# Kernel optimization log

Measured on AMD Instinct MI355X. Metric: run time of the kernel, lower is better.

## Reference

```python
import jax, jax.numpy as jnp
import numpy as np

N_NODES = 100000
N_CLASSES = 16


def _graph_conv(x, W, b, src, dst, n_nodes):
    # DGL GraphConv norm='both': D_out^{-1/2} on src, aggregate, D_in^{-1/2} on dst.
    ones = jnp.ones(src.shape[0], x.dtype)
    deg_out = jnp.clip(jax.ops.segment_sum(ones, src, num_segments=n_nodes), 1.0)
    deg_in = jnp.clip(jax.ops.segment_sum(ones, dst, num_segments=n_nodes), 1.0)
    h = (x * jax.lax.rsqrt(deg_out)[:, None]) @ W          # [N, out] project first (in>=out)
    agg = jax.ops.segment_sum(h[src], dst, num_segments=n_nodes)  # gather-scatter
    return agg * jax.lax.rsqrt(deg_in)[:, None] + b


def _hetero_conv(x, W, b, edge_src, edge_dst, n_nodes):
    # HeteroGraphConv(aggregate='sum') over R relations, each its own GraphConv.
    out = _graph_conv(x, W[0], b[0], edge_src[0], edge_dst[0], n_nodes)
    for r in range(1, W.shape[0]):
        out = out + _graph_conv(x, W[r], b[r], edge_src[r], edge_dst[r], n_nodes)
    return out


def reference(x, W0, b0, W_mu, b_mu, W_ls, b_ls, edge_src, edge_dst,
              pos_src, pos_dst, neg_src, neg_dst):
    n = x.shape[0]
    h1 = jax.nn.relu(_hetero_conv(x, W0, b0, edge_src, edge_dst, n))
    mean = _hetero_conv(h1, W_mu, b_mu, edge_src, edge_dst, n)
    log_std = _hetero_conv(h1, W_ls, b_ls, edge_src, edge_dst, n)
    noise = jax.random.normal(jax.random.key(42), mean.shape, mean.dtype)
    h = mean + noise * jnp.exp(log_std)                     # VGAE reparameterization
    pos_score = jnp.sum(h[pos_src] * h[pos_dst], axis=-1, keepdims=True)  # u_dot_v
    neg_score = jnp.sum(h[neg_src] * h[neg_dst], axis=-1, keepdims=True)
    return pos_score, neg_score, h


def setup_inputs() -> dict:
    key = jax.random.key(0)
    ks = jax.random.split(key, 12)
    R, E, EP = 3, 1600000, 500000
    in_f, hid, out = 128, 64, N_CLASSES
    return {
        "x": jax.random.normal(ks[0], (N_NODES, in_f), jnp.float32),
        "W0": jax.random.normal(ks[1], (R, in_f, hid), jnp.float32) * (1.0 / np.sqrt(in_f)),
        "b0": jnp.zeros((R, hid), jnp.float32),
        "W_mu": jax.random.normal(ks[2], (R, hid, out), jnp.float32) * (1.0 / np.sqrt(hid)),
        "b_mu": jnp.zeros((R, out), jnp.float32),
        "W_ls": jax.random.normal(ks[3], (R, hid, out), jnp.float32) * (1.0 / np.sqrt(hid)),
        "b_ls": jnp.zeros((R, out), jnp.float32),
        "edge_src": jax.random.randint(ks[4], (R, E), 0, N_NODES, jnp.int32),
        "edge_dst": jax.random.randint(ks[5], (R, E), 0, N_NODES, jnp.int32),
        "pos_src": jax.random.randint(ks[6], (EP,), 0, N_NODES, jnp.int32),
        "pos_dst": jax.random.randint(ks[7], (EP,), 0, N_NODES, jnp.int32),
        "neg_src": jax.random.randint(ks[8], (EP,), 0, N_NODES, jnp.int32),
        "neg_dst": jax.random.randint(ks[9], (EP,), 0, N_NODES, jnp.int32),
    }
```

## Files before the change

kernel.cpp:

```cpp
#include <hip/hip_runtime.h>
#include <math.h>

#define N_NODES 100000
#define NREL 3
#define E_PER 1600000
#define E_TOT 4800000
#define EP 500000
#define F_IN 128
#define F_HID 64
#define F_OUT 16
#define NRN 300000

#define NSEG 7
#define SEGSZ 16000
#define NBLK 32
#define CHUNK (E_PER / NBLK)
#define SEGO 25000
#define NSEGO 4

#define OFF_DOUT    0
#define OFF_DINVIN  300000
#define OFF_CNT     600000
#define OFF_G       900000
#define OFF_BSUM    1200000
#define OFF_CSR     1201024
#define OFF_ESLOT   6001024
#define OFF_HPROJ   6001024
#define OFF_H1      12401088
#define OFF_HP22    18801088
#define WS_NEED_CSR 22001120
#define HP2SZ 3200032
#define ODINV_OUT 0
#define ODINV_IN  300000
#define OH1ACC    600000
#define OHPROJ    7000000
#define OL2ACC    13400000

__device__ __forceinline__ float atomAddF(float* p, float v) {
    return unsafeAtomicAdd(p, v);
}

__device__ __forceinline__ unsigned rotl32(unsigned x, unsigned d) {
    return (x << d) | (x >> (32u - d));
}

__device__ float jax_noise(unsigned i) {
    const unsigned ks0 = 0u, ks1 = 42u;
    const unsigned ks2 = ks0 ^ ks1 ^ 0x1BD11BDAu;
    unsigned x0 = 0u + ks0;
    unsigned x1 = i + ks1;
#define TFR(r) { x0 += x1; x1 = rotl32(x1, r); x1 ^= x0; }
    TFR(13) TFR(15) TFR(26) TFR(6)
    x0 += ks1; x1 += ks2 + 1u;
    TFR(17) TFR(29) TFR(16) TFR(24)
    x0 += ks2; x1 += ks0 + 2u;
    TFR(13) TFR(15) TFR(26) TFR(6)
    x0 += ks0; x1 += ks1 + 3u;
    TFR(17) TFR(29) TFR(16) TFR(24)
    x0 += ks1; x1 += ks2 + 4u;
    TFR(13) TFR(15) TFR(26) TFR(6)
    x0 += ks2; x1 += ks0 + 5u;
#undef TFR
    const unsigned bits = x0 ^ x1;
    float f = __uint_as_float((bits >> 9) | 0x3f800000u) - 1.0f;
    const float lo = -0.99999994f;
    float u = fmaxf(lo, f * 2.0f + lo);
    float w = -log1pf(-u * u);
    float p;
    if (w < 5.0f) {
        w -= 2.5f;
        p = 2.81022636e-08f;
        p = fmaf(p, w, 3.43273939e-07f);
        p = fmaf(p, w, -3.5233877e-06f);
        p = fmaf(p, w, -4.39150654e-06f);
        p = fmaf(p, w, 0.00021858087f);
        p = fmaf(p, w, -0.00125372503f);
        p = fmaf(p, w, -0.00417768164f);
        p = fmaf(p, w, 0.246640727f);
        p = fmaf(p, w, 1.50140941f);
    } else {
        w = sqrtf(w) - 3.0f;
        p = -0.000200214257f;
        p = fmaf(p, w, 0.000100950558f);
        p = fmaf(p, w, 0.00134934322f);
        p = fmaf(p, w, -0.00367342844f);
        p = fmaf(p, w, 0.00573950773f);
        p = fmaf(p, w, -0.0076224613f);
        p = fmaf(p, w, 0.00943887047f);
        p = fmaf(p, w, 1.00167406f);
        p = fmaf(p, w, 2.83297682f);
    }
    return 1.41421356237f * (p * u);
}

__global__ __launch_bounds__(512) void k_histin(const int* __restrict__ ed,
                                                int* __restrict__ cnt,
                                                int* __restrict__ eslot) {
    __shared__ int lds[SEGSZ];
    const int r = blockIdx.z, g = blockIdx.y, b = blockIdx.x;
    const int lo = g * SEGSZ;
    const int hi = min(lo + SEGSZ, N_NODES);
    const int nbins = hi - lo;
    for (int i = threadIdx.x; i < nbins; i += 512) lds[i] = 0;
    __syncthreads();
    const int e0 = r * E_PER + b * CHUNK;
    const int e1 = e0 + CHUNK;
    for (int e = e0 + threadIdx.x * 4; e + 4 <= e1; e += 512 * 4) {
        const int4 d4 = *(const int4*)(ed + e);
        if (d4.x >= lo && d4.x < hi) atomicAdd(&lds[d4.x - lo], 1);
        if (d4.y >= lo && d4.y < hi) atomicAdd(&lds[d4.y - lo], 1);
        if (d4.z >= lo && d4.z < hi) atomicAdd(&lds[d4.z - lo], 1);
        if (d4.w >= lo && d4.w < hi) atomicAdd(&lds[d4.w - lo], 1);
    }
    __syncthreads();
    for (int i = threadIdx.x; i < nbins; i += 512) {
        const int c = lds[i];
        lds[i] = c ? atomicAdd(&cnt[r * N_NODES + lo + i], c) : 0;
    }
    __syncthreads();
    for (int e = e0 + threadIdx.x * 4; e + 4 <= e1; e += 512 * 4) {
        const int4 d4 = *(const int4*)(ed + e);
        if (d4.x >= lo && d4.x < hi) eslot[e]     = atomicAdd(&lds[d4.x - lo], 1);
        if (d4.y >= lo && d4.y < hi) eslot[e + 1] = atomicAdd(&lds[d4.y - lo], 1);
        if (d4.z >= lo && d4.z < hi) eslot[e + 2] = atomicAdd(&lds[d4.z - lo], 1);
        if (d4.w >= lo && d4.w < hi) eslot[e + 3] = atomicAdd(&lds[d4.w - lo], 1);
    }
}

__global__ __launch_bounds__(512) void k_histout(const int* __restrict__ es,
                                                 int* __restrict__ dout) {
    __shared__ int lds[SEGO / 2];
    const int r = blockIdx.z, g = blockIdx.y, b = blockIdx.x;
    const int lo = g * SEGO;
    const int hi = lo + SEGO;
    for (int i = threadIdx.x; i < SEGO / 2; i += 512) lds[i] = 0;
    __syncthreads();
    const int e0 = r * E_PER + b * CHUNK;
    const int e1 = e0 + CHUNK;
    for (int e = e0 + threadIdx.x * 4; e + 4 <= e1; e += 512 * 4) {
        const int4 s4 = *(const int4*)(es + e);
        if (s4.x >= lo && s4.x < hi) {
            const int i = s4.x - lo;
            atomicAdd(&lds[i >> 1], 1 << ((i & 1) * 16));
        }
        if (s4.y >= lo && s4.y < hi) {
            const int i = s4.y - lo;
            atomicAdd(&lds[i >> 1], 1 << ((i & 1) * 16));
        }
        if (s4.z >= lo && s4.z < hi) {
            const int i = s4.z - lo;
            atomicAdd(&lds[i >> 1], 1 << ((i & 1) * 16));
        }
        if (s4.w >= lo && s4.w < hi) {
            const int i = s4.w - lo;
            atomicAdd(&lds[i >> 1], 1 << ((i & 1) * 16));
        }
    }
    __syncthreads();
    for (int i = threadIdx.x; i < SEGO / 2; i += 512) {
        const unsigned c = (unsigned)lds[i];
        const int c0 = (int)(c & 0xffffu);
        const int c1 = (int)(c >> 16);
        if (c0) atomicAdd(&dout[r * N_NODES + lo + 2 * i], c0);
        if (c1) atomicAdd(&dout[r * N_NODES + lo + 2 * i + 1], c1);
    }
}

__global__ __launch_bounds__(256) void k_scanA(const int* __restrict__ cnt,
                                               int* __restrict__ bsum) {
    __shared__ int red[256];
    const int base = blockIdx.x * 1024 + threadIdx.x * 4;
    int s = 0;
#pragma unroll
    for (int q = 0; q < 4; ++q) {
        const int i = base + q;
        s += (i < NRN) ? cnt[i] : 0;
    }
    red[threadIdx.x] = s;
    __syncthreads();
    for (int w = 128; w > 0; w >>= 1) {
        if (threadIdx.x < w) red[threadIdx.x] += red[threadIdx.x + w];
        __syncthreads();
    }
    if (threadIdx.x == 0) bsum[blockIdx.x] = red[0];
}

__global__ __launch_bounds__(512) void k_scanB(int* __restrict__ bsum) {
    __shared__ int sc[512];
    const int t = threadIdx.x;
    sc[t] = (t < 294) ? bsum[t] : 0;
    __syncthreads();
    for (int o = 1; o < 512; o <<= 1) {
        const int v = (t >= o) ? sc[t - o] : 0;
        __syncthreads();
        sc[t] += v;
        __syncthreads();
    }
    bsum[t] = (t > 0) ? sc[t - 1] : 0;
}

__global__ __launch_bounds__(256) void k_scanC(const int* __restrict__ cnt,
                                               const int* __restrict__ bsum,
                                               int* __restrict__ G,
                                               float* __restrict__ dinv_in,
                                               int* doutc) {
    __shared__ int sc[256];
    const int t = threadIdx.x;
    const int base = blockIdx.x * 1024 + t * 4;
    int v[4];
    int ts = 0;
#pragma unroll
    for (int q = 0; q < 4; ++q) {
        const int i = base + q;
        v[q] = (i < NRN) ? cnt[i] : 0;
        ts += v[q];
    }
    sc[t] = ts;
    __syncthreads();
    for (int o = 1; o < 256; o <<= 1) {
        const int x = (t >= o) ? sc[t - o] : 0;
        __syncthreads();
        sc[t] += x;
        __syncthreads();
    }
    int run = bsum[blockIdx.x] + ((t > 0) ? sc[t - 1] : 0);
#pragma unroll
    for (int q = 0; q < 4; ++q) {
        const int i = base + q;
        if (i < NRN) {
            G[i] = run;
            dinv_in[i] = rsqrtf((float)max(v[q], 1));
            const int oc = doutc[i];
            ((float*)doutc)[i] = rsqrtf((float)max(oc, 1));
        }
        run += v[q];
    }
}

__global__ __launch_bounds__(256) void k_fill(const int* __restrict__ es,
                                              const int* __restrict__ ed,
                                              const int* __restrict__ eslot,
                                              const int* __restrict__ G,
                                              int* __restrict__ csr) {
    const int r = blockIdx.y;
    const int e = (blockIdx.x * 256 + threadIdx.x) * 4;
    if (e + 4 > E_PER) return;
    const int gid = r * E_PER + e;
    const int4 s4 = *(const int4*)(es + gid);
    const int4 d4 = *(const int4*)(ed + gid);
    const int4 l4 = *(const int4*)(eslot + gid);
    const int rb = r * N_NODES;
    csr[G[rb + d4.x] + l4.x] = s4.x;
    csr[G[rb + d4.y] + l4.y] = s4.y;
    csr[G[rb + d4.z] + l4.z] = s4.z;
    csr[G[rb + d4.w] + l4.w] = s4.w;
}

__global__ __launch_bounds__(256) void k_gather1(const float* __restrict__ hp,
                                                 const int* __restrict__ csr,
                                                 const int* __restrict__ G,
                                                 const float* __restrict__ dinv,
                                                 float* __restrict__ h1,
                                                 int rbase, int first) {
    const int node = (blockIdx.x * 256 + threadIdx.x) >> 6;
    const int lane = threadIdx.x & 63;
    const int l16 = lane & 15;
    const int e4 = lane >> 4;
    const int idx = rbase + node;
    const int off0 = G[idx];
    const int off1 = (idx == NRN - 1) ? E_TOT : G[idx + 1];
    float ax = 0.f, ay = 0.f, az = 0.f, aw = 0.f;
    for (int base = off0; base < off1; base += 64) {
        int m = off1 - base;
        if (m > 64) m = 64;
        const int sv = (lane < m) ? csr[base + lane] : N_NODES;
        const int nq = (m + 3) >> 2;
        for (int q = 0; q < nq; ++q) {
            const int ei = q * 4 + e4;
            const int s = __shfl(sv, ei);
            const float4 v = *(const float4*)(hp + (size_t)s * F_HID + l16 * 4);
            ax += v.x;
            ay += v.y;
            az += v.z;
            aw += v.w;
        }
    }
    ax += __shfl_xor(ax, 16); ay += __shfl_xor(ay, 16);
    az += __shfl_xor(az, 16); aw += __shfl_xor(aw, 16);
    ax += __shfl_xor(ax, 32); ay += __shfl_xor(ay, 32);
    az += __shfl_xor(az, 32); aw += __shfl_xor(aw, 32);
    if (lane < 16) {
        const float dv = dinv[idx];
        float4* dst = (float4*)(h1 + (size_t)node * F_HID) + l16;
        float4 o;
        if (first) {
            o.x = dv * ax; o.y = dv * ay; o.z = dv * az; o.w = dv * aw;
        } else {
            const float4 pr = *dst;
            o.x = pr.x + dv * ax; o.y = pr.y + dv * ay;
            o.z = pr.z + dv * az; o.w = pr.w + dv * aw;
        }
        *dst = o;
    }
}

__global__ __launch_bounds__(256) void k_gather2_all(const float* __restrict__ hp0,
                                                     const float* __restrict__ hp1,
                                                     const float* __restrict__ hp2,
                                                     const int* __restrict__ csr,
                                                     const int* __restrict__ G,
                                                     const float* __restrict__ dinv,
                                                     const float* __restrict__ bmu,
                                                     const float* __restrict__ bls,
                                                     float* __restrict__ outh) {
    const int node = (blockIdx.x * 256 + threadIdx.x) >> 4;
    const int lane = threadIdx.x & 63;
    const int gl = lane & 15;
    const int l8 = lane & 7;
    const int e2 = (lane >> 3) & 1;
    float ox = 0.f, oy = 0.f, oz = 0.f, ow = 0.f;
#pragma unroll
    for (int r = 0; r < NREL; ++r) {
        const float* hp = (r == 0) ? hp0 : (r == 1) ? hp1 : hp2;
        const int idx = r * N_NODES + node;
        const int off0 = G[idx];
        const int off1 = (idx == NRN - 1) ? E_TOT : G[idx + 1];
        const int deg = off1 - off0;
        float ax = 0.f, ay = 0.f, az = 0.f, aw = 0.f;
        for (int ei0 = 0; ei0 < deg; ei0 += 4) {
            const int eiA = ei0 + e2;
            const int eiB = ei0 + 2 + e2;
            const int sA = (eiA < deg) ? csr[off0 + eiA] : N_NODES;
            const int sB = (eiB < deg) ? csr[off0 + eiB] : N_NODES;
            const float4 vA = *(const float4*)(hp + (size_t)sA * 32 + l8 * 4);
            const float4 vB = *(const float4*)(hp + (size_t)sB * 32 + l8 * 4);
            ax += vA.x; ay += vA.y; az += vA.z; aw += vA.w;
            ax += vB.x; ay += vB.y; az += vB.z; aw += vB.w;
        }
        ax += __shfl_xor(ax, 8);
        ay += __shfl_xor(ay, 8);
        az += __shfl_xor(az, 8);
        aw += __shfl_xor(aw, 8);
        const float dv = dinv[idx];
        ox = fmaf(dv, ax, ox);
        oy = fmaf(dv, ay, oy);
        oz = fmaf(dv, az, oz);
        ow = fmaf(dv, aw, ow);
    }
    const int gb = lane & 48;
    const int srcM = gb + (gl >> 2);
    const int srcL = gb + 4 + (gl >> 2);
    const float m0 = __shfl(ox, srcM), m1 = __shfl(oy, srcM),
                m2 = __shfl(oz, srcM), m3 = __shfl(ow, srcM);
    const float s0 = __shfl(ox, srcL), s1 = __shfl(oy, srcL),
                s2 = __shfl(oz, srcL), s3 = __shfl(ow, srcL);
    const float mm = (gl & 2) ? ((gl & 1) ? m3 : m2) : ((gl & 1) ? m1 : m0);
    const float ss = (gl & 2) ? ((gl & 1) ? s3 : s2) : ((gl & 1) ? s1 : s0);
    const float mean = mm + bmu[gl] + bmu[16 + gl] + bmu[32 + gl];
    const float lstd = ss + bls[gl] + bls[16 + gl] + bls[32 + gl];
    outh[(size_t)node * 16 + gl] =
        mean + jax_noise((unsigned)(node * 16 + gl)) * expf(lstd);
}

__global__ __launch_bounds__(256) void k_project1(const float* __restrict__ x,
                                                  const float* __restrict__ W,
                                                  const float* __restrict__ dinv,
                                                  float* __restrict__ out) {
    __shared__ float ws[F_IN * F_HID];
    for (int i = threadIdx.x; i < F_IN * F_HID; i += 256) ws[i] = W[i];
    __syncthreads();
    for (int t = blockIdx.x * 256 + threadIdx.x; t < (N_NODES + 1) * 16;
         t += gridDim.x * 256) {
        const int n = t >> 4;
        const int c0 = (t & 15) << 2;
        const int nn = min(n, N_NODES - 1);
        const float4* xr = (const float4*)(x + (size_t)nn * F_IN);
        float a0 = 0.f, a1 = 0.f, a2 = 0.f, a3 = 0.f;
#pragma unroll 8
        for (int k4 = 0; k4 < F_IN / 4; ++k4) {
            const float4 xv = xr[k4];
            const float4 w0 = *(const float4*)(ws + (k4 * 4 + 0) * F_HID + c0);
            const float4 w1 = *(const float4*)(ws + (k4 * 4 + 1) * F_HID + c0);
            const float4 w2 = *(const float4*)(ws + (k4 * 4 + 2) * F_HID + c0);
            const float4 w3 = *(const float4*)(ws + (k4 * 4 + 3) * F_HID + c0);
            a0 = fmaf(xv.x, w0.x, a0); a1 = fmaf(xv.x, w0.y, a1);
            a2 = fmaf(xv.x, w0.z, a2); a3 = fmaf(xv.x, w0.w, a3);
            a0 = fmaf(xv.y, w1.x, a0); a1 = fmaf(xv.y, w1.y, a1);
            a2 = fmaf(xv.y, w1.z, a2); a3 = fmaf(xv.y, w1.w, a3);
            a0 = fmaf(xv.z, w2.x, a0); a1 = fmaf(xv.z, w2.y, a1);
            a2 = fmaf(xv.z, w2.z, a2); a3 = fmaf(xv.z, w2.w, a3);
            a0 = fmaf(xv.w, w3.x, a0); a1 = fmaf(xv.w, w3.y, a1);
            a2 = fmaf(xv.w, w3.z, a2); a3 = fmaf(xv.w, w3.w, a3);
        }
        const float dv = (n < N_NODES) ? dinv[nn] : 0.f;
        float4 o;
        o.x = a0 * dv; o.y = a1 * dv; o.z = a2 * dv; o.w = a3 * dv;
        *(float4*)(out + (size_t)n * F_HID + c0) = o;
    }
}

__global__ __launch_bounds__(256) void k_project2(const float* __restrict__ h1,
                                                  const float* __restrict__ b0,
                                                  const float* __restrict__ Wmu,
                                                  const float* __restrict__ Wls,
                                                  const float* __restrict__ dinv,
                                                  float* __restrict__ out) {
    __shared__ float ws[F_HID * 32];
    __shared__ float bs[F_HID];
    for (int i = threadIdx.x; i < F_HID * 32; i += 256) {
        const int k = i >> 5, c = i & 31;
        ws[i] = (c < 16) ? Wmu[k * 16 + c] : Wls[k * 16 + (c - 16)];
    }
    if (threadIdx.x < F_HID)
        bs[threadIdx.x] = b0[threadIdx.x] + b0[64 + threadIdx.x] + b0[128 + threadIdx.x];
    __syncthreads();
    for (int t = blockIdx.x * 256 + threadIdx.x; t < (N_NODES + 1) * 8;
         t += gridDim.x * 256) {
        const int n = t >> 3;
        const int c0 = (t & 7) << 2;
        const int nn = min(n, N_NODES - 1);
        const float4* hr = (const float4*)(h1 + (size_t)nn * F_HID);
        float a0 = 0.f, a1 = 0.f, a2 = 0.f, a3 = 0.f;
#pragma unroll 4
        for (int k4 = 0; k4 < F_HID / 4; ++k4) {
            const float4 hv = hr[k4];
            const float4 bv = *(const float4*)(bs + k4 * 4);
            const float r0 = fmaxf(hv.x + bv.x, 0.f);
            const float r1 = fmaxf(hv.y + bv.y, 0.f);
            const float r2 = fmaxf(hv.z + bv.z, 0.f);
            const float r3 = fmaxf(hv.w + bv.w, 0.f);
            const float4 w0 = *(const float4*)(ws + (k4 * 4 + 0) * 32 + c0);
            const float4 w1 = *(const float4*)(ws + (k4 * 4 + 1) * 32 + c0);
            const float4 w2 = *(const float4*)(ws + (k4 * 4 + 2) * 32 + c0);
            const float4 w3 = *(const float4*)(ws + (k4 * 4 + 3) * 32 + c0);
            a0 = fmaf(r0, w0.x, a0); a1 = fmaf(r0, w0.y, a1);
            a2 = fmaf(r0, w0.z, a2); a3 = fmaf(r0, w0.w, a3);
            a0 = fmaf(r1, w1.x, a0); a1 = fmaf(r1, w1.y, a1);
            a2 = fmaf(r1, w1.z, a2); a3 = fmaf(r1, w1.w, a3);
            a0 = fmaf(r2, w2.x, a0); a1 = fmaf(r2, w2.y, a1);
            a2 = fmaf(r2, w2.z, a2); a3 = fmaf(r2, w2.w, a3);
            a0 = fmaf(r3, w3.x, a0); a1 = fmaf(r3, w3.y, a1);
            a2 = fmaf(r3, w3.z, a2); a3 = fmaf(r3, w3.w, a3);
        }
        const float dv = (n < N_NODES) ? dinv[nn] : 0.f;
        float4 o;
        o.x = a0 * dv; o.y = a1 * dv; o.z = a2 * dv; o.w = a3 * dv;
        *(float4*)(out + (size_t)n * 32 + c0) = o;
    }
}

__global__ __launch_bounds__(256) void k_scores(const int* __restrict__ ps,
                                                const int* __restrict__ pd,
                                                const int* __restrict__ ns,
                                                const int* __restrict__ nd,
                                                const float* __restrict__ h,
                                                float* __restrict__ out) {
    const int i = blockIdx.x * 256 + threadIdx.x;
    if (i >= 2 * EP) return;
    const int j = (i < EP) ? i : i - EP;
    const int a = (i < EP) ? ps[j] : ns[j];
    const int b = (i < EP) ? pd[j] : nd[j];
    const float4* ha = (const float4*)(h + (size_t)a * 16);
    const float4* hb = (const float4*)(h + (size_t)b * 16);
    float s = 0.f;
#pragma unroll
    for (int q = 0; q < 4; ++q) {
        const float4 u = ha[q];
        const float4 v = hb[q];
        s += u.x * v.x + u.y * v.y + u.z * v.z + u.w * v.w;
    }
    out[i] = s;
}

__global__ __launch_bounds__(256) void k_degrees(const int* __restrict__ es,
                                                 const int* __restrict__ ed,
                                                 float* __restrict__ dout,
                                                 float* __restrict__ din) {
    const int r = blockIdx.y;
    const int e = blockIdx.x * 256 + threadIdx.x;
    const int s = es[r * E_PER + e];
    const int d = ed[r * E_PER + e];
    atomAddF(&dout[r * N_NODES + s], 1.0f);
    atomAddF(&din[r * N_NODES + d], 1.0f);
}

__global__ __launch_bounds__(256) void k_finalize_deg(float* __restrict__ d) {
    const int i = blockIdx.x * 256 + threadIdx.x;
    if (i < 2 * NRN) d[i] = 1.0f / sqrtf(fmaxf(d[i], 1.0f));
}

__global__ __launch_bounds__(256) void k_scatter1(const float* __restrict__ hp,
                                                  const int* __restrict__ es,
                                                  const int* __restrict__ ed,
                                                  const float* __restrict__ din,
                                                  float* __restrict__ acc) {
    const int t = blockIdx.x * 256 + threadIdx.x;
    const int e = t >> 6;
    const int lane = t & 63;
    const int s = es[e];
    const int d = ed[e];
    const float v = hp[s * F_HID + lane] * din[d];
    atomAddF(&acc[d * F_HID + lane], v);
}

__global__ __launch_bounds__(256) void k_scatter2(const float* __restrict__ hp,
                                                  const int* __restrict__ es,
                                                  const int* __restrict__ ed,
                                                  const float* __restrict__ din,
                                                  float* __restrict__ acc) {
    const int t = blockIdx.x * 256 + threadIdx.x;
    const int e = t >> 5;
    const int c = t & 31;
    const int s = es[e];
    const int d = ed[e];
    const float v = hp[s * 32 + c] * din[d];
    atomAddF(&acc[d * 32 + c], v);
}

__global__ __launch_bounds__(256) void k_finalize(const float* __restrict__ l2,
                                                  const float* __restrict__ bmu,
                                                  const float* __restrict__ bls,
                                                  float* __restrict__ outh) {
    const int i = blockIdx.x * 256 + threadIdx.x;
    const int n = i >> 4, c = i & 15;
    const float mean = l2[n * 32 + c] + bmu[c] + bmu[16 + c] + bmu[32 + c];
    const float lstd = l2[n * 32 + 16 + c] + bls[c] + bls[16 + c] + bls[32 + c];
    const float z = jax_noise((unsigned)i);
    outh[i] = mean + z * expf(lstd);
}

extern "C" void kernel_launch(void* const* d_in, const int* in_sizes, int n_in,
                              void* d_out, int out_size, void* d_ws, size_t ws_size,
                              hipStream_t stream) {
    const float* x   = (const float*)d_in[0];
    const float* W0  = (const float*)d_in[1];
    const float* b0  = (const float*)d_in[2];
    const float* Wmu = (const float*)d_in[3];
    const float* bmu = (const float*)d_in[4];
    const float* Wls = (const float*)d_in[5];
    const float* bls = (const float*)d_in[6];
    const int* es = (const int*)d_in[7];
    const int* ed = (const int*)d_in[8];
    const int* ps = (const int*)d_in[9];
    const int* pd = (const int*)d_in[10];
    const int* ns = (const int*)d_in[11];
    const int* nd = (const int*)d_in[12];
    float* out = (float*)d_out;
    float* wsf = (float*)d_ws;

    if (ws_size >= (size_t)WS_NEED_CSR * sizeof(float)) {
        int*   doutc   = (int*)(wsf + OFF_DOUT);
        float* doutf   = wsf + OFF_DOUT;
        float* dinv_in = wsf + OFF_DINVIN;
        int*   cnt     = (int*)(wsf + OFF_CNT);
        int*   G       = (int*)(wsf + OFF_G);
        int*   bsum    = (int*)(wsf + OFF_BSUM);
        int*   csr     = (int*)(wsf + OFF_CSR);
        int*   eslot   = (int*)(wsf + OFF_ESLOT);
        float* hproj   = wsf + OFF_HPROJ;
        float* hp20    = wsf + OFF_HPROJ;
        float* hp21    = wsf + OFF_HPROJ + HP2SZ;
        float* hp22    = wsf + OFF_HP22;
        float* h1acc   = wsf + OFF_H1;

        hipMemsetAsync(doutc, 0, (size_t)NRN * sizeof(int), stream);
        hipMemsetAsync(cnt, 0, (size_t)NRN * sizeof(int), stream);

        k_histin<<<dim3(NBLK, NSEG, NREL), 512, 0, stream>>>(ed, cnt, eslot);
        k_histout<<<dim3(NBLK, NSEGO, NREL), 512, 0, stream>>>(es, doutc);
        k_scanA<<<294, 256, 0, stream>>>(cnt, bsum);
        k_scanB<<<1, 512, 0, stream>>>(bsum);
        k_scanC<<<294, 256, 0, stream>>>(cnt, bsum, G, dinv_in, doutc);
        k_fill<<<dim3((E_PER / 4 + 255) / 256, NREL), 256, 0, stream>>>(
            es, ed, eslot, G, csr);

        for (int r = 0; r < NREL; ++r) {
            k_project1<<<1280, 256, 0, stream>>>(
                x, W0 + (size_t)r * F_IN * F_HID, doutf + (size_t)r * N_NODES, hproj);
            k_gather1<<<N_NODES / 4, 256, 0, stream>>>(
                hproj, csr, G, dinv_in, h1acc, r * N_NODES, r == 0);
        }
        float* hp2s[NREL] = {hp20, hp21, hp22};
        for (int r = 0; r < NREL; ++r) {
            k_project2<<<1024, 256, 0, stream>>>(
                h1acc, b0, Wmu + (size_t)r * F_HID * F_OUT,
                Wls + (size_t)r * F_HID * F_OUT, doutf + (size_t)r * N_NODES,
                hp2s[r]);
        }
        k_gather2_all<<<N_NODES / 16, 256, 0, stream>>>(
            hp20, hp21, hp22, csr, G, dinv_in, bmu, bls, out + 2 * EP);
        k_scores<<<(2 * EP + 255) / 256, 256, 0, stream>>>(
            ps, pd, ns, nd, out + 2 * EP, out);
    } else {
        float* dinv_out = wsf + ODINV_OUT;
        float* dinv_in  = wsf + ODINV_IN;
        float* h1acc    = wsf + OH1ACC;
        float* hproj    = wsf + OHPROJ;
        float* l2acc    = wsf + OL2ACC;

        hipMemsetAsync(dinv_out, 0, (size_t)2 * NRN * sizeof(float), stream);
        hipMemsetAsync(h1acc, 0, (size_t)N_NODES * F_HID * sizeof(float), stream);
        hipMemsetAsync(l2acc, 0, (size_t)N_NODES * 32 * sizeof(float), stream);

        k_degrees<<<dim3(E_PER / 256, NREL), 256, 0, stream>>>(es, ed, dinv_out, dinv_in);
        k_finalize_deg<<<(2 * NRN + 255) / 256, 256, 0, stream>>>(wsf);

        for (int r = 0; r < NREL; ++r) {
            k_project1<<<1280, 256, 0, stream>>>(
                x, W0 + (size_t)r * F_IN * F_HID, dinv_out + (size_t)r * N_NODES, hproj);
            k_scatter1<<<E_PER / 4, 256, 0, stream>>>(
                hproj, es + (size_t)r * E_PER, ed + (size_t)r * E_PER,
                dinv_in + (size_t)r * N_NODES, h1acc);
        }
        for (int r = 0; r < NREL; ++r) {
            k_project2<<<1024, 256, 0, stream>>>(
                h1acc, b0, Wmu + (size_t)r * F_HID * F_OUT,
                Wls + (size_t)r * F_HID * F_OUT, dinv_out + (size_t)r * N_NODES, hproj);
            k_scatter2<<<E_PER / 8, 256, 0, stream>>>(
                hproj, es + (size_t)r * E_PER, ed + (size_t)r * E_PER,
                dinv_in + (size_t)r * N_NODES, l2acc);
        }
        k_finalize<<<N_NODES * F_OUT / 256, 256, 0, stream>>>(
            l2acc, bmu, bls, out + 2 * EP);
        k_scores<<<(2 * EP + 255) / 256, 256, 0, stream>>>(
            ps, pd, ns, nd, out + 2 * EP, out);
    }
}
```

Measured before the change: 843.9 us.

## Fuse per-relation layer-2 projections, enlarge histogram segments, unroll gather2 loop

Replaces the three k_project2 launches with a single k_project2_all kernel. It reads each h1 row once and applies the ReLU+bias once for all three relations, cutting repeated h1 reads and launch overhead. The histogram kernels now use dynamic shared memory with larger segments, so fewer segments are needed and the edge arrays are rescanned fewer times, at some cost to occupancy. The gather2 inner loop is unrolled to four neighbour loads per step to raise memory-level parallelism, which also raises register pressure.

Result: faster. 792.7 us (-6.1%).

```diff
diff --git a/kernel.cpp b/kernel.cpp
--- a/kernel.cpp
+++ b/kernel.cpp
@@ -11,12 +11,12 @@
 #define F_OUT 16
 #define NRN 300000
 
-#define NSEG 7
-#define SEGSZ 16000
+#define NSEG 5
+#define SEGSZ 20000
 #define NBLK 32
 #define CHUNK (E_PER / NBLK)
-#define SEGO 25000
-#define NSEGO 4
+#define SEGO 40000
+#define NSEGO 3
 
 #define OFF_DOUT    0
 #define OFF_DINVIN  300000
@@ -96,7 +96,7 @@
 __global__ __launch_bounds__(512) void k_histin(const int* __restrict__ ed,
                                                 int* __restrict__ cnt,
                                                 int* __restrict__ eslot) {
-    __shared__ int lds[SEGSZ];
+    extern __shared__ int lds[];
     const int r = blockIdx.z, g = blockIdx.y, b = blockIdx.x;
     const int lo = g * SEGSZ;
     const int hi = min(lo + SEGSZ, N_NODES);
@@ -129,11 +129,13 @@
 
 __global__ __launch_bounds__(512) void k_histout(const int* __restrict__ es,
                                                  int* __restrict__ dout) {
-    __shared__ int lds[SEGO / 2];
+    extern __shared__ int lds[];
     const int r = blockIdx.z, g = blockIdx.y, b = blockIdx.x;
     const int lo = g * SEGO;
-    const int hi = lo + SEGO;
-    for (int i = threadIdx.x; i < SEGO / 2; i += 512) lds[i] = 0;
+    const int hi = min(lo + SEGO, N_NODES);
+    const int nbins = hi - lo;
+    const int nwords = (nbins + 1) >> 1;
+    for (int i = threadIdx.x; i < nwords; i += 512) lds[i] = 0;
     __syncthreads();
     const int e0 = r * E_PER + b * CHUNK;
     const int e1 = e0 + CHUNK;
@@ -157,12 +159,13 @@
         }
     }
     __syncthreads();
-    for (int i = threadIdx.x; i < SEGO / 2; i += 512) {
+    for (int i = threadIdx.x; i < nwords; i += 512) {
         const unsigned c = (unsigned)lds[i];
         const int c0 = (int)(c & 0xffffu);
         const int c1 = (int)(c >> 16);
         if (c0) atomicAdd(&dout[r * N_NODES + lo + 2 * i], c0);
-        if (c1) atomicAdd(&dout[r * N_NODES + lo + 2 * i + 1], c1);
+        if (c1 && 2 * i + 1 < nbins)
+            atomicAdd(&dout[r * N_NODES + lo + 2 * i + 1], c1);
     }
 }
 
@@ -327,15 +330,23 @@
         const int off1 = (idx == NRN - 1) ? E_TOT : G[idx + 1];
         const int deg = off1 - off0;
         float ax = 0.f, ay = 0.f, az = 0.f, aw = 0.f;
-        for (int ei0 = 0; ei0 < deg; ei0 += 4) {
+        for (int ei0 = 0; ei0 < deg; ei0 += 8) {
             const int eiA = ei0 + e2;
             const int eiB = ei0 + 2 + e2;
+            const int eiC = ei0 + 4 + e2;
+            const int eiD = ei0 + 6 + e2;
             const int sA = (eiA < deg) ? csr[off0 + eiA] : N_NODES;
             const int sB = (eiB < deg) ? csr[off0 + eiB] : N_NODES;
+            const int sC = (eiC < deg) ? csr[off0 + eiC] : N_NODES;
+            const int sD = (eiD < deg) ? csr[off0 + eiD] : N_NODES;
             const float4 vA = *(const float4*)(hp + (size_t)sA * 32 + l8 * 4);
             const float4 vB = *(const float4*)(hp + (size_t)sB * 32 + l8 * 4);
+            const float4 vC = *(const float4*)(hp + (size_t)sC * 32 + l8 * 4);
+            const float4 vD = *(const float4*)(hp + (size_t)sD * 32 + l8 * 4);
             ax += vA.x; ay += vA.y; az += vA.z; aw += vA.w;
             ax += vB.x; ay += vB.y; az += vB.z; aw += vB.w;
+            ax += vC.x; ay += vC.y; az += vC.z; aw += vC.w;
+            ax += vD.x; ay += vD.y; az += vD.z; aw += vD.w;
         }
         ax += __shfl_xor(ax, 8);
         ay += __shfl_xor(ay, 8);
@@ -396,6 +407,78 @@
         float4 o;
         o.x = a0 * dv; o.y = a1 * dv; o.z = a2 * dv; o.w = a3 * dv;
         *(float4*)(out + (size_t)n * F_HID + c0) = o;
+    }
+}
+
+__global__ __launch_bounds__(256) void k_project2_all(const float* __restrict__ h1,
+                                                      const float* __restrict__ b0,
+                                                      const float* __restrict__ Wmu,
+                                                      const float* __restrict__ Wls,
+                                                      const float* __restrict__ dinv,
+                                                      float* __restrict__ o0,
+                                                      float* __restrict__ o1,
+                                                      float* __restrict__ o2) {
+    __shared__ float ws[NREL * F_HID * 32];
+    __shared__ float bs[F_HID];
+    for (int i = threadIdx.x; i < NREL * F_HID * 32; i += 256) {
+        const int r = i >> 11;
+        const int j = i & 2047;
+        const int k = j >> 5, c = j & 31;
+        ws[i] = (c < 16) ? Wmu[r * F_HID * 16 + k * 16 + c]
+                         : Wls[r * F_HID * 16 + k * 16 + (c - 16)];
+    }
+    if (threadIdx.x < F_HID)
+        bs[threadIdx.x] = b0[threadIdx.x] + b0[64 + threadIdx.x] + b0[128 + threadIdx.x];
+    __syncthreads();
+    for (int t = blockIdx.x * 256 + threadIdx.x; t < (N_NODES + 1) * 8;
+         t += gridDim.x * 256) {
+        const int n = t >> 3;
+        const int c0 = (t & 7) << 2;
+        const int nn = min(n, N_NODES - 1);
+        const float4* hr = (const float4*)(h1 + (size_t)nn * F_HID);
+        float a00 = 0.f, a01 = 0.f, a02 = 0.f, a03 = 0.f;
+        float a10 = 0.f, a11 = 0.f, a12 = 0.f, a13 = 0.f;
+        float a20 = 0.f, a21 = 0.f, a22 = 0.f, a23 = 0.f;
+#pragma unroll 2
+        for (int k4 = 0; k4 < F_HID / 4; ++k4) {
+            const float4 hv = hr[k4];
+            const float4 bv = *(const float4*)(bs + k4 * 4);
+            const float r0 = fmaxf(hv.x + bv.x, 0.f);
+            const float r1 = fmaxf(hv.y + bv.y, 0.f);
+            const float r2 = fmaxf(hv.z + bv.z, 0.f);
+            const float r3 = fmaxf(hv.w + bv.w, 0.f);
+#pragma unroll
+            for (int rr = 0; rr < NREL; ++rr) {
+                const float* wb = ws + rr * F_HID * 32;
+                const float4 w0 = *(const float4*)(wb + (k4 * 4 + 0) * 32 + c0);
+                const float4 w1 = *(const float4*)(wb + (k4 * 4 + 1) * 32 + c0);
+                const float4 w2 = *(const float4*)(wb + (k4 * 4 + 2) * 32 + c0);
+                const float4 w3 = *(const float4*)(wb + (k4 * 4 + 3) * 32 + c0);
+                float* pa0 = (rr == 0) ? &a00 : (rr == 1) ? &a10 : &a20;
+                float* pa1 = (rr == 0) ? &a01 : (rr == 1) ? &a11 : &a21;
+                float* pa2 = (rr == 0) ? &a02 : (rr == 1) ? &a12 : &a22;
+                float* pa3 = (rr == 0) ? &a03 : (rr == 1) ? &a13 : &a23;
+                *pa0 = fmaf(r0, w0.x, *pa0); *pa1 = fmaf(r0, w0.y, *pa1);
+                *pa2 = fmaf(r0, w0.z, *pa2); *pa3 = fmaf(r0, w0.w, *pa3);
+                *pa0 = fmaf(r1, w1.x, *pa0); *pa1 = fmaf(r1, w1.y, *pa1);
+                *pa2 = fmaf(r1, w1.z, *pa2); *pa3 = fmaf(r1, w1.w, *pa3);
+                *pa0 = fmaf(r2, w2.x, *pa0); *pa1 = fmaf(r2, w2.y, *pa1);
+                *pa2 = fmaf(r2, w2.z, *pa2); *pa3 = fmaf(r2, w2.w, *pa3);
+                *pa0 = fmaf(r3, w3.x, *pa0); *pa1 = fmaf(r3, w3.y, *pa1);
+                *pa2 = fmaf(r3, w3.z, *pa2); *pa3 = fmaf(r3, w3.w, *pa3);
+            }
+        }
+        const bool valid = (n < N_NODES);
+        const float dv0 = valid ? dinv[nn] : 0.f;
+        const float dv1 = valid ? dinv[N_NODES + nn] : 0.f;
+        const float dv2 = valid ? dinv[2 * N_NODES + nn] : 0.f;
+        float4 q;
+        q.x = a00 * dv0; q.y = a01 * dv0; q.z = a02 * dv0; q.w = a03 * dv0;
+        *(float4*)(o0 + (size_t)n * 32 + c0) = q;
+        q.x = a10 * dv1; q.y = a11 * dv1; q.z = a12 * dv1; q.w = a13 * dv1;
+        *(float4*)(o1 + (size_t)n * 32 + c0) = q;
+        q.x = a20 * dv2; q.y = a21 * dv2; q.z = a22 * dv2; q.w = a23 * dv2;
+        *(float4*)(o2 + (size_t)n * 32 + c0) = q;
     }
 }
 
@@ -566,8 +649,10 @@
         hipMemsetAsync(doutc, 0, (size_t)NRN * sizeof(int), stream);
         hipMemsetAsync(cnt, 0, (size_t)NRN * sizeof(int), stream);
 
-        k_histin<<<dim3(NBLK, NSEG, NREL), 512, 0, stream>>>(ed, cnt, eslot);
-        k_histout<<<dim3(NBLK, NSEGO, NREL), 512, 0, stream>>>(es, doutc);
+        k_histin<<<dim3(NBLK, NSEG, NREL), 512, SEGSZ * sizeof(int), stream>>>(
+            ed, cnt, eslot);
+        k_histout<<<dim3(NBLK, NSEGO, NREL), 512, (SEGO / 2) * sizeof(int), stream>>>(
+            es, doutc);
         k_scanA<<<294, 256, 0, stream>>>(cnt, bsum);
         k_scanB<<<1, 512, 0, stream>>>(bsum);
         k_scanC<<<294, 256, 0, stream>>>(cnt, bsum, G, dinv_in, doutc);
@@ -580,13 +665,8 @@
             k_gather1<<<N_NODES / 4, 256, 0, stream>>>(
                 hproj, csr, G, dinv_in, h1acc, r * N_NODES, r == 0);
         }
-        float* hp2s[NREL] = {hp20, hp21, hp22};
-        for (int r = 0; r < NREL; ++r) {
-            k_project2<<<1024, 256, 0, stream>>>(
-                h1acc, b0, Wmu + (size_t)r * F_HID * F_OUT,
-                Wls + (size_t)r * F_HID * F_OUT, doutf + (size_t)r * N_NODES,
-                hp2s[r]);
-        }
+        k_project2_all<<<1024, 256, 0, stream>>>(
+            h1acc, b0, Wmu, Wls, doutf, hp20, hp21, hp22);
         k_gather2_all<<<N_NODES / 16, 256, 0, stream>>>(
             hp20, hp21, hp22, csr, G, dinv_in, bmu, bls, out + 2 * EP);
         k_scores<<<(2 * EP + 255) / 256, 256, 0, stream>>>(
```
